# Optimization experiments

Hardware: AMD Instinct MI355X
Metric: run time of the kernel (lower is better)

Reference implementation:

```python
import jax, jax.numpy as jnp
import numpy as np

B, N, D, H = 4, 1024, 512, 8
DH = D // H  # per-head dim for V and for each of the two Q/K halves
LAM = 0.5


def setup_inputs() -> dict:
    key = jax.random.key(0)
    ks = jax.random.split(key, 7)
    s = 0.02
    return {
        "x": jax.random.normal(ks[0], (B, N, D), dtype=jnp.float32),
        "Wq": jax.random.normal(ks[1], (D, 2 * D), dtype=jnp.float32) * s,
        "bq": jax.random.normal(ks[2], (2 * D,), dtype=jnp.float32) * s,
        "Wk": jax.random.normal(ks[3], (D, 2 * D), dtype=jnp.float32) * s,
        "bk": jax.random.normal(ks[4], (2 * D,), dtype=jnp.float32) * s,
        "Wv": jax.random.normal(ks[5], (D, D), dtype=jnp.float32) * s,
        "bv": jax.random.normal(ks[6], (D,), dtype=jnp.float32) * s,
    }


def reference(x, Wq, bq, Wk, bk, Wv, bv):
    b, n, d = x.shape
    q = (x @ Wq + bq).reshape(b, n, H, 2 * DH).transpose(0, 2, 1, 3)  # [B,H,N,2*DH]
    k = (x @ Wk + bk).reshape(b, n, H, 2 * DH).transpose(0, 2, 1, 3)
    v = (x @ Wv + bv).reshape(b, n, H, DH).transpose(0, 2, 1, 3)      # [B,H,N,DH]
    q1, q2 = q[..., :DH], q[..., DH:]
    k1, k2 = k[..., :DH], k[..., DH:]
    scale = 1.0 / jnp.sqrt(jnp.float32(DH))
    a1 = jax.nn.softmax(jnp.einsum("bhqd,bhkd->bhqk", q1, k1) * scale, axis=-1)
    a2 = jax.nn.softmax(jnp.einsum("bhqd,bhkd->bhqk", q2, k2) * scale, axis=-1)
    attn = a1 - LAM * a2                                              # [B,H,N,N]
    out = jnp.einsum("bhqk,bhkd->bhqd", attn, v)                      # [B,H,N,DH]
    return out.transpose(0, 2, 1, 3).reshape(b, n, d)
```

## Files before the change

kernel.cpp:

```cpp
#include <hip/hip_runtime.h>
#include <hip/hip_bf16.h>

typedef unsigned short u16;
typedef unsigned int u32;
typedef short s16x8 __attribute__((ext_vector_type(8)));
typedef short s16x4 __attribute__((ext_vector_type(4)));
typedef float f32x4 __attribute__((ext_vector_type(4)));
typedef float f32x16 __attribute__((ext_vector_type(16)));

__device__ inline u16 f2bf(float f) {
  union { float f; unsigned int u; } v; v.f = f;
  unsigned int r = v.u + 0x7fffu + ((v.u >> 16) & 1u);
  return (u16)(r >> 16);
}

__device__ __forceinline__ u32 cvt_pk_bf16(float lo, float hi) {
  u32 r;
  asm("v_cvt_pk_bf16_f32 %0, %1, %2" : "=v"(r) : "v"(lo), "v"(hi));
  return r;
}

__device__ __forceinline__ void g2lds16(const u16* g, u16* l) {
  __builtin_amdgcn_global_load_lds((const __attribute__((address_space(1))) void*)g,
                                   (__attribute__((address_space(3))) void*)l, 16, 0, 0);
}

__global__ __launch_bounds__(256) void prep_kernel(const float* __restrict__ x, u16* __restrict__ xb,
                                                   const float* __restrict__ Wq,
                                                   const float* __restrict__ Wk,
                                                   const float* __restrict__ Wv,
                                                   u16* __restrict__ wt) {
  if (blockIdx.x >= 40) {
    int i = (((blockIdx.x - 40) * 8 + blockIdx.y) * 256 + threadIdx.x) * 8;
    float4 a = *(const float4*)(x + i);
    float4 b = *(const float4*)(x + i + 4);
    s16x8 o;
    o[0] = (short)f2bf(a.x); o[1] = (short)f2bf(a.y);
    o[2] = (short)f2bf(a.z); o[3] = (short)f2bf(a.w);
    o[4] = (short)f2bf(b.x); o[5] = (short)f2bf(b.y);
    o[6] = (short)f2bf(b.z); o[7] = (short)f2bf(b.w);
    *(s16x8*)(xb + i) = o;
    return;
  }
  __shared__ float tile[64][65];
  int jg = blockIdx.x * 64;
  const float* src; int C, j0;
  if (jg < 1024)      { src = Wq; C = 1024; j0 = jg; }
  else if (jg < 2048) { src = Wk; C = 1024; j0 = jg - 1024; }
  else                { src = Wv; C = 512;  j0 = jg - 2048; }
  int k0 = blockIdx.y * 64;
  int tx = threadIdx.x % 64, ty4 = threadIdx.x / 64;
#pragma unroll
  for (int p = 0; p < 16; ++p) {
    int r = p * 4 + ty4;
    tile[r][tx] = src[(size_t)(k0 + r) * C + j0 + tx];
  }
  __syncthreads();
#pragma unroll
  for (int p = 0; p < 16; ++p) {
    int r = p * 4 + ty4;
    wt[(size_t)(jg + r) * 512 + k0 + tx] = f2bf(tile[tx][r]);
  }
}

__global__ __launch_bounds__(256, 2) void gemm_qkv(const u16* __restrict__ xb, const u16* __restrict__ wt,
                                                   const float* __restrict__ bq, const float* __restrict__ bk,
                                                   const float* __restrict__ bv,
                                                   u16* __restrict__ qa, u16* __restrict__ ka,
                                                   u16* __restrict__ va) {
  __shared__ __align__(16) u16 As[128 * 64];
  __shared__ __align__(16) u16 Bs[128 * 64];
  int m0 = blockIdx.x * 128, j0 = blockIdx.y * 128;
  bool isV = (j0 >= 2048);
  int tid = threadIdx.x;
  int w = tid >> 6, lane = tid & 63, quad = lane >> 4, l16 = lane & 15;
  int wr = (w >> 1) * 64, wc = (w & 1) * 64;

  int srow[4], scol[4], sbase[4];
#pragma unroll
  for (int it = 0; it < 4; ++it) {
    int s = it * 256 + tid;
    srow[it] = s >> 3;
    scol[it] = (s & 7) ^ ((s >> 3) & 7);
    sbase[it] = (s & ~63) * 8;
  }

  f32x4 acc[4][4];
#pragma unroll
  for (int i = 0; i < 4; ++i)
#pragma unroll
    for (int j = 0; j < 4; ++j)
#pragma unroll
      for (int r = 0; r < 4; ++r) acc[i][j][r] = 0.f;

  for (int kk = 0; kk < 8; ++kk) {
    int k0 = kk * 64;
    __syncthreads();
#pragma unroll
    for (int it = 0; it < 4; ++it) {
      g2lds16(xb + (size_t)(m0 + srow[it]) * 512 + k0 + scol[it] * 8, &As[sbase[it]]);
      g2lds16(wt + (size_t)(j0 + srow[it]) * 512 + k0 + scol[it] * 8, &Bs[sbase[it]]);
    }
    __syncthreads();
#pragma unroll
    for (int kb = 0; kb < 2; ++kb) {
      s16x8 af[4], bfr[4];
#pragma unroll
      for (int rb = 0; rb < 4; ++rb) {
        int row = wr + rb * 16 + l16;
        af[rb] = *(const s16x8*)(&As[row * 64 + (((kb * 4 + quad) ^ (row & 7)) * 8)]);
      }
#pragma unroll
      for (int cb = 0; cb < 4; ++cb) {
        int row = wc + cb * 16 + l16;
        bfr[cb] = *(const s16x8*)(&Bs[row * 64 + (((kb * 4 + quad) ^ (row & 7)) * 8)]);
      }
      if (isV) {
#pragma unroll
        for (int rb = 0; rb < 4; ++rb)
#pragma unroll
          for (int cb = 0; cb < 4; ++cb)
            acc[rb][cb] = __builtin_amdgcn_mfma_f32_16x16x32_bf16(bfr[cb], af[rb], acc[rb][cb], 0, 0, 0);
      } else {
#pragma unroll
        for (int rb = 0; rb < 4; ++rb)
#pragma unroll
          for (int cb = 0; cb < 4; ++cb)
            acc[rb][cb] = __builtin_amdgcn_mfma_f32_16x16x32_bf16(af[rb], bfr[cb], acc[rb][cb], 0, 0, 0);
      }
    }
  }

  if (isV) {
#pragma unroll
    for (int cb = 0; cb < 4; ++cb) {
#pragma unroll
      for (int rb = 0; rb < 4; ++rb) {
        int m = m0 + wr + rb * 16 + l16;
        int bidx = m >> 10, n = m & 1023;
#pragma unroll
        for (int r = 0; r < 4; ++r) {
          int jj = j0 - 2048 + wc + cb * 16 + quad * 4 + r;
          int h = jj >> 6, d = jj & 63;
          float bias = bv[jj];
          va[((size_t)((bidx * 8 + h) * 64 + d)) * 1024 + n] = f2bf(acc[rb][cb][r] + bias);
        }
      }
    }
  } else {
#pragma unroll
    for (int cb = 0; cb < 4; ++cb) {
      int j = j0 + wc + cb * 16 + l16;
      bool isQ = (j < 1024);
      float bias = isQ ? bq[j] : bk[j - 1024];
#pragma unroll
      for (int rb = 0; rb < 4; ++rb) {
#pragma unroll
        for (int r = 0; r < 4; ++r) {
          int m = m0 + wr + rb * 16 + quad * 4 + r;
          int bidx = m >> 10, n = m & 1023;
          float val = acc[rb][cb][r] + bias;
          u16 o = f2bf(isQ ? val * 0.18033688f : val);
          if (isQ) {
            int h = j >> 7, r2 = j & 127;
            qa[((size_t)((bidx * 8 + h) * 1024 + n)) * 128 + r2] = o;
          } else {
            int jj = j - 1024, h = jj >> 7, r2 = jj & 127;
            ka[((size_t)((bidx * 8 + h) * 1024 + n)) * 128 + r2] = o;
          }
        }
      }
    }
  }
}

__global__ __launch_bounds__(256, 2) void attn_kernel(const u16* __restrict__ qa, const u16* __restrict__ ka,
                                                      const u16* __restrict__ va, float* __restrict__ out) {
  __shared__ __align__(16) u16 smem[40960];
  int bh = blockIdx.x, b = bh >> 3, h = bh & 7;
  int q0 = blockIdx.y * 64;
  int tid = threadIdx.x, w = tid >> 6, lane = tid & 63;
  int l32 = lane & 31, hi = lane >> 5;
  int team = w >> 1, wq = w & 1, t = tid & 127;
  u16* hb = smem + team * 20480;
  u16* const KbA = hb;
  u16* const KbB = hb + 8192;
  u16* const Vsb = hb + 16384;

  const u16* qrow = qa + (size_t)(bh * 1024 + q0 + wq * 32 + l32) * 128;
  s16x8 qf[2][4];
#pragma unroll
  for (int hh = 0; hh < 2; ++hh)
#pragma unroll
    for (int kb = 0; kb < 4; ++kb)
      qf[hh][kb] = *(const s16x8*)(qrow + 64 * hh + 16 * kb + 8 * hi);

  f32x16 O1[2], O2[2];
#pragma unroll
  for (int d = 0; d < 2; ++d)
#pragma unroll
    for (int r = 0; r < 16; ++r) { O1[d][r] = 0.f; O2[d][r] = 0.f; }
  float ds1 = 0.f, ds2 = 0.f;

  int r0 = t >> 4, c0 = t & 15;
  int rv = t >> 3, cv = (t & 7) ^ ((t >> 3) & 7);
  const u16* kgbase = ka + (size_t)bh * 1024 * 128;
  const u16* vgbase = va + (size_t)bh * 64 * 1024;
  int nbase = team * 512;

  auto stageK = [&](int n0, u16* Kd) {
#pragma unroll
    for (int it = 0; it < 8; ++it) {
      int row = r0 + 8 * it;
      int chunk = c0 ^ (row & 15);
      g2lds16(kgbase + (size_t)(n0 + row) * 128 + chunk * 8, Kd + (it * 128 + (t & 64)) * 8);
    }
  };
  auto stageV = [&](int n0) {
#pragma unroll
    for (int it = 0; it < 4; ++it)
      g2lds16(vgbase + (size_t)(rv + 16 * it) * 1024 + n0 + cv * 8, Vsb + (it * 128 + (t & 64)) * 8);
  };

  stageK(nbase, KbA);
  stageV(nbase);
  __syncthreads();

  for (int kt = 0; kt < 8; ++kt) {
    u16* const KsC = (kt & 1) ? KbB : KbA;
    u16* const KsN = (kt & 1) ? KbA : KbB;
    if (kt < 7) stageK(nbase + (kt + 1) * 64, KsN);

    s16x8 pa[2][4];
#pragma unroll
    for (int hh = 0; hh < 2; ++hh) {
      f32x16 sv[2];
#pragma unroll
      for (int nb = 0; nb < 2; ++nb)
#pragma unroll
        for (int r = 0; r < 16; ++r) sv[nb][r] = 0.f;
#pragma unroll
      for (int nb = 0; nb < 2; ++nb) {
        int row = nb * 32 + l32, rbase = row * 128, rx15 = row & 15;
#pragma unroll
        for (int kb = 0; kb < 4; ++kb) {
          s16x8 kf = *(const s16x8*)(&KsC[rbase + (((8 * hh + 2 * kb + hi) ^ rx15) * 8)]);
          sv[nb] = __builtin_amdgcn_mfma_f32_32x32x16_bf16(kf, qf[hh][kb], sv[nb], 0, 0, 0);
        }
      }
      float dsl = 0.f;
#pragma unroll
      for (int s = 0; s < 4; ++s) {
        float e[8];
#pragma unroll
        for (int j = 0; j < 8; ++j) {
          e[j] = __builtin_exp2f(sv[s >> 1][(s & 1) * 8 + j]);
          dsl += e[j];
        }
        union { u32 wd[4]; s16x8 v; } u;
        u.wd[0] = cvt_pk_bf16(e[0], e[1]);
        u.wd[1] = cvt_pk_bf16(e[2], e[3]);
        u.wd[2] = cvt_pk_bf16(e[4], e[5]);
        u.wd[3] = cvt_pk_bf16(e[6], e[7]);
        pa[hh][s] = u.v;
      }
      if (hh == 0) ds1 += dsl; else ds2 += dsl;
    }

    s16x8 vB[4][2];
#pragma unroll
    for (int dblk = 0; dblk < 2; ++dblk) {
      int row = dblk * 32 + l32, rbase = row * 64, rx = row & 7;
#pragma unroll
      for (int s = 0; s < 4; ++s) {
        union { s16x4 hl[2]; s16x8 v; } u;
        u.hl[0] = *(const s16x4*)(&Vsb[rbase + (((2 * s) ^ rx) * 8) + 4 * hi]);
        u.hl[1] = *(const s16x4*)(&Vsb[rbase + (((2 * s + 1) ^ rx) * 8) + 4 * hi]);
        vB[s][dblk] = u.v;
      }
    }

    asm volatile("s_waitcnt lgkmcnt(0)\n\ts_barrier" ::: "memory");
    if (kt < 7) stageV(nbase + (kt + 1) * 64);

#pragma unroll
    for (int s = 0; s < 4; ++s)
#pragma unroll
      for (int dblk = 0; dblk < 2; ++dblk) {
        O1[dblk] = __builtin_amdgcn_mfma_f32_32x32x16_bf16(pa[0][s], vB[s][dblk], O1[dblk], 0, 0, 0);
        O2[dblk] = __builtin_amdgcn_mfma_f32_32x32x16_bf16(pa[1][s], vB[s][dblk], O2[dblk], 0, 0, 0);
      }

    __syncthreads();
  }

  float* scr = (float*)smem;
  int mbase = wq * 4224 + lane;
  if (team == 1) {
#pragma unroll
    for (int r = 0; r < 16; ++r) {
      scr[mbase + r * 64]        = O1[0][r];
      scr[mbase + (16 + r) * 64] = O1[1][r];
      scr[mbase + (32 + r) * 64] = O2[0][r];
      scr[mbase + (48 + r) * 64] = O2[1][r];
    }
    scr[mbase + 64 * 64] = ds1;
    scr[mbase + 65 * 64] = ds2;
  }
  __syncthreads();
  if (team == 0) {
#pragma unroll
    for (int r = 0; r < 16; ++r) {
      O1[0][r] += scr[mbase + r * 64];
      O1[1][r] += scr[mbase + (16 + r) * 64];
      O2[0][r] += scr[mbase + (32 + r) * 64];
      O2[1][r] += scr[mbase + (48 + r) * 64];
    }
    ds1 += scr[mbase + 64 * 64];
    ds2 += scr[mbase + 65 * 64];
    ds1 += __shfl_xor(ds1, 32, 64);
    ds2 += __shfl_xor(ds2, 32, 64);
    float inv1 = 1.0f / ds1, inv2 = 1.0f / ds2;
#pragma unroll
    for (int r = 0; r < 16; ++r) {
      int iq = (r & 3) + 8 * (r >> 2) + 4 * hi;
      float i1 = __shfl(inv1, iq, 64);
      float i2 = __shfl(inv2, iq, 64);
      size_t orow = (size_t)(b * 1024 + q0 + wq * 32 + iq) * 512 + h * 64 + l32;
      out[orow]      = O1[0][r] * i1 - 0.5f * O2[0][r] * i2;
      out[orow + 32] = O1[1][r] * i1 - 0.5f * O2[1][r] * i2;
    }
  }
}

extern "C" void kernel_launch(void* const* d_in, const int* in_sizes, int n_in,
                              void* d_out, int out_size, void* d_ws, size_t ws_size,
                              hipStream_t stream) {
  (void)in_sizes; (void)n_in; (void)out_size; (void)ws_size;
  const float* x  = (const float*)d_in[0];
  const float* Wq = (const float*)d_in[1];
  const float* bq = (const float*)d_in[2];
  const float* Wk = (const float*)d_in[3];
  const float* bk = (const float*)d_in[4];
  const float* Wv = (const float*)d_in[5];
  const float* bv = (const float*)d_in[6];
  float* out = (float*)d_out;

  char* ws = (char*)d_ws;
  u16* xb = (u16*)(ws);
  u16* wt = (u16*)(ws + 4194304);
  u16* qa = (u16*)(ws + 6815744);
  u16* ka = (u16*)(ws + 15204352);
  u16* va = (u16*)(ws + 23592960);

  prep_kernel<<<dim3(168, 8), 256, 0, stream>>>(x, xb, Wq, Wk, Wv, wt);
  gemm_qkv<<<dim3(32, 20), 256, 0, stream>>>(xb, wt, bq, bk, bv, qa, ka, va);
  attn_kernel<<<dim3(32, 16), 256, 0, stream>>>(qa, ka, va, out);
}
```

Before: 132.9 us.

## Halve key tile to 32 and double-buffer V alongside K

Shrinks the per-iteration key tile from 64 to 32 rows, so each team now runs 16 iterations. Both K and V get double buffers and are prefetched together for the next tile, which removes the mid-loop barrier and the separate V staging. LDS use per block falls from 80KB to 48KB, which may let more blocks fit per CU. The cost is twice as many loop iterations and syncthreads, with less MFMA work between each barrier.

```diff
diff --git a/kernel.cpp b/kernel.cpp
--- a/kernel.cpp
+++ b/kernel.cpp
@@ -176,16 +176,17 @@
 
 __global__ __launch_bounds__(256, 2) void attn_kernel(const u16* __restrict__ qa, const u16* __restrict__ ka,
                                                       const u16* __restrict__ va, float* __restrict__ out) {
-  __shared__ __align__(16) u16 smem[40960];
+  __shared__ __align__(16) u16 smem[24576];
   int bh = blockIdx.x, b = bh >> 3, h = bh & 7;
   int q0 = blockIdx.y * 64;
   int tid = threadIdx.x, w = tid >> 6, lane = tid & 63;
   int l32 = lane & 31, hi = lane >> 5;
   int team = w >> 1, wq = w & 1, t = tid & 127;
-  u16* hb = smem + team * 20480;
+  u16* hb = smem + team * 12288;
   u16* const KbA = hb;
-  u16* const KbB = hb + 8192;
-  u16* const Vsb = hb + 16384;
+  u16* const KbB = hb + 4096;
+  u16* const VbA = hb + 8192;
+  u16* const VbB = hb + 10240;
 
   const u16* qrow = qa + (size_t)(bh * 1024 + q0 + wq * 32 + l32) * 128;
   s16x8 qf[2][4];
@@ -203,58 +204,61 @@
   float ds1 = 0.f, ds2 = 0.f;
 
   int r0 = t >> 4, c0 = t & 15;
-  int rv = t >> 3, cv = (t & 7) ^ ((t >> 3) & 7);
+  int rv = t >> 2, cv = (t & 3) ^ ((t >> 3) & 3);
   const u16* kgbase = ka + (size_t)bh * 1024 * 128;
   const u16* vgbase = va + (size_t)bh * 64 * 1024;
   int nbase = team * 512;
 
   auto stageK = [&](int n0, u16* Kd) {
 #pragma unroll
-    for (int it = 0; it < 8; ++it) {
-      int row = r0 + 8 * it;
-      int chunk = c0 ^ (row & 15);
-      g2lds16(kgbase + (size_t)(n0 + row) * 128 + chunk * 8, Kd + (it * 128 + (t & 64)) * 8);
+    for (int it = 0; it < 4; ++it) {
+      int row = it * 8 + r0;
+      g2lds16(kgbase + (size_t)(n0 + row) * 128 + (c0 ^ (row & 15)) * 8,
+              Kd + (it * 128 + (t & 64)) * 8);
     }
   };
-  auto stageV = [&](int n0) {
-#pragma unroll
-    for (int it = 0; it < 4; ++it)
-      g2lds16(vgbase + (size_t)(rv + 16 * it) * 1024 + n0 + cv * 8, Vsb + (it * 128 + (t & 64)) * 8);
+  auto stageV = [&](int n0, u16* Vd) {
+#pragma unroll
+    for (int it = 0; it < 2; ++it) {
+      int row = it * 32 + rv;
+      g2lds16(vgbase + (size_t)row * 1024 + n0 + cv * 8,
+              Vd + (it * 128 + (t & 64)) * 8);
+    }
   };
 
   stageK(nbase, KbA);
-  stageV(nbase);
+  stageV(nbase, VbA);
   __syncthreads();
 
-  for (int kt = 0; kt < 8; ++kt) {
-    u16* const KsC = (kt & 1) ? KbB : KbA;
-    u16* const KsN = (kt & 1) ? KbA : KbB;
-    if (kt < 7) stageK(nbase + (kt + 1) * 64, KsN);
-
-    s16x8 pa[2][4];
+  for (int kt = 0; kt < 16; ++kt) {
+    int cur = kt & 1;
+    u16* const KsC = cur ? KbB : KbA;
+    u16* const VsC = cur ? VbB : VbA;
+    if (kt < 15) {
+      int n1 = nbase + (kt + 1) * 32;
+      stageK(n1, cur ? KbA : KbB);
+      stageV(n1, cur ? VbA : VbB);
+    }
+
+    s16x8 pa[2][2];
 #pragma unroll
     for (int hh = 0; hh < 2; ++hh) {
-      f32x16 sv[2];
-#pragma unroll
-      for (int nb = 0; nb < 2; ++nb)
-#pragma unroll
-        for (int r = 0; r < 16; ++r) sv[nb][r] = 0.f;
-#pragma unroll
-      for (int nb = 0; nb < 2; ++nb) {
-        int row = nb * 32 + l32, rbase = row * 128, rx15 = row & 15;
-#pragma unroll
-        for (int kb = 0; kb < 4; ++kb) {
-          s16x8 kf = *(const s16x8*)(&KsC[rbase + (((8 * hh + 2 * kb + hi) ^ rx15) * 8)]);
-          sv[nb] = __builtin_amdgcn_mfma_f32_32x32x16_bf16(kf, qf[hh][kb], sv[nb], 0, 0, 0);
-        }
+      f32x16 sv;
+#pragma unroll
+      for (int r = 0; r < 16; ++r) sv[r] = 0.f;
+      int rbase = l32 * 128, rx15 = l32 & 15;
+#pragma unroll
+      for (int kb = 0; kb < 4; ++kb) {
+        s16x8 kf = *(const s16x8*)(&KsC[rbase + (((8 * hh + 2 * kb + hi) ^ rx15) * 8)]);
+        sv = __builtin_amdgcn_mfma_f32_32x32x16_bf16(kf, qf[hh][kb], sv, 0, 0, 0);
       }
       float dsl = 0.f;
 #pragma unroll
-      for (int s = 0; s < 4; ++s) {
+      for (int s = 0; s < 2; ++s) {
         float e[8];
 #pragma unroll
         for (int j = 0; j < 8; ++j) {
-          e[j] = __builtin_exp2f(sv[s >> 1][(s & 1) * 8 + j]);
+          e[j] = __builtin_exp2f(sv[s * 8 + j]);
           dsl += e[j];
         }
         union { u32 wd[4]; s16x8 v; } u;
@@ -267,24 +271,21 @@
       if (hh == 0) ds1 += dsl; else ds2 += dsl;
     }
 
-    s16x8 vB[4][2];
+    s16x8 vB[2][2];
 #pragma unroll
     for (int dblk = 0; dblk < 2; ++dblk) {
-      int row = dblk * 32 + l32, rbase = row * 64, rx = row & 7;
-#pragma unroll
-      for (int s = 0; s < 4; ++s) {
+      int row = dblk * 32 + l32, rbase = row * 32, rx = (row >> 1) & 3;
+#pragma unroll
+      for (int s = 0; s < 2; ++s) {
         union { s16x4 hl[2]; s16x8 v; } u;
-        u.hl[0] = *(const s16x4*)(&Vsb[rbase + (((2 * s) ^ rx) * 8) + 4 * hi]);
-        u.hl[1] = *(const s16x4*)(&Vsb[rbase + (((2 * s + 1) ^ rx) * 8) + 4 * hi]);
+        u.hl[0] = *(const s16x4*)(&VsC[rbase + (((2 * s) ^ rx) * 8) + 4 * hi]);
+        u.hl[1] = *(const s16x4*)(&VsC[rbase + (((2 * s + 1) ^ rx) * 8) + 4 * hi]);
         vB[s][dblk] = u.v;
       }
     }
 
-    asm volatile("s_waitcnt lgkmcnt(0)\n\ts_barrier" ::: "memory");
-    if (kt < 7) stageV(nbase + (kt + 1) * 64);
-
-#pragma unroll
-    for (int s = 0; s < 4; ++s)
+#pragma unroll
+    for (int s = 0; s < 2; ++s)
 #pragma unroll
       for (int dblk = 0; dblk < 2; ++dblk) {
         O1[dblk] = __builtin_amdgcn_mfma_f32_32x32x16_bf16(pa[0][s], vB[s][dblk], O1[dblk], 0, 0, 0);
```

Result: faster. 128.3 us (-3.5%).
